# Kernel optimization log

Measured on AMD Instinct MI355X. Metric: run time of the kernel, lower is better.

Reference implementation:

```python
import jax, jax.numpy as jnp
import numpy as np

B, T, C = 2, 2048, 2048
H = 16
D = C // H  # head_size = 128
ROPE_BASE = 10000.0


def _rope_cos_sin(seq_len, dim, dtype=jnp.float32):
    # torchtune RotaryPositionalEmbeddings: interleaved pair rotation
    inv_freq = 1.0 / (ROPE_BASE ** (jnp.arange(0, dim, 2, dtype=jnp.float32) / dim))  # [D/2]
    ang = jnp.arange(seq_len, dtype=jnp.float32)[:, None] * inv_freq[None, :]  # [T, D/2]
    return jnp.cos(ang).astype(dtype), jnp.sin(ang).astype(dtype)


def _apply_rope(x, cos, sin):
    # x: [B, T, H, D]; rotate interleaved pairs (even, odd)
    x1 = x[..., 0::2]
    x2 = x[..., 1::2]
    c = cos[None, :, None, :]
    s = sin[None, :, None, :]
    out = jnp.stack([x1 * c - x2 * s, x1 * s + x2 * c], axis=-1)  # [B,T,H,D/2,2]
    return out.reshape(x.shape)


def setup_inputs() -> dict:
    key = jax.random.key(0)
    ks = jax.random.split(key, 5)
    scale = 1.0 / np.sqrt(C)
    return {
        "x": jax.random.normal(ks[0], (B, T, C), jnp.float32),
        "W_attn": jax.random.normal(ks[1], (C, 3 * C), jnp.float32) * scale,
        "b_attn": jax.random.normal(ks[2], (3 * C,), jnp.float32) * 0.01,
        "W_proj": jax.random.normal(ks[3], (C, C), jnp.float32) * scale,
        "b_proj": jax.random.normal(ks[4], (C,), jnp.float32) * 0.01,
    }


def reference(x, W_attn, b_attn, W_proj, b_proj):
    b, t, c = x.shape
    qkv = x @ W_attn + b_attn                      # [B,T,3C]
    q, k, v = jnp.split(qkv, 3, axis=-1)
    q = q.reshape(b, t, H, D)
    k = k.reshape(b, t, H, D)
    v = v.reshape(b, t, H, D)
    cos, sin = _rope_cos_sin(t, D, x.dtype)
    q = _apply_rope(q, cos, sin)
    k = _apply_rope(k, cos, sin)
    # [B,H,T,D]
    q = q.transpose(0, 2, 1, 3)
    k = k.transpose(0, 2, 1, 3)
    v = v.transpose(0, 2, 1, 3)
    scores = jnp.einsum("bhqd,bhkd->bhqk", q, k) / jnp.sqrt(jnp.asarray(D, x.dtype))
    causal = jnp.tril(jnp.ones((t, t), dtype=bool))  # [T,T]
    scores = jnp.where(causal[None, None], scores, jnp.asarray(-jnp.inf, scores.dtype))
    probs = jax.nn.softmax(scores, axis=-1)
    out = jnp.einsum("bhqk,bhkd->bhqd", probs, v)  # [B,H,T,D]
    out = out.transpose(0, 2, 1, 3).reshape(b, t, c)
    return out @ W_proj + b_proj
```

## Files before the change

kernel.cpp:

```cpp
#include <hip/hip_runtime.h>
#include <hip/hip_bf16.h>
#include <math.h>

#define B_ 2
#define T_ 2048
#define C_ 2048
#define H_ 16
#define D_ 128
#define M_ (B_ * T_)
#define N3C (3 * C_)

typedef __attribute__((ext_vector_type(8))) short v8s;
typedef __attribute__((ext_vector_type(4))) float v4f;

typedef const __attribute__((address_space(1))) void* gas_t;
typedef __attribute__((address_space(3))) void* las_t;

__device__ __forceinline__ void gl16(const void* g, void* l) {
  __builtin_amdgcn_global_load_lds((gas_t)g, (las_t)l, 16, 0, 0);
}
__device__ __forceinline__ v8s ldv(const unsigned short* p) { return *(const v8s*)p; }

__device__ inline unsigned short f2bf(float f) {
  unsigned u = __builtin_bit_cast(unsigned, f);
  u += 0x7FFFu + ((u >> 16) & 1u);
  return (unsigned short)(u >> 16);
}
__device__ inline float bf2f(unsigned short h) {
  unsigned u = (unsigned)h << 16;
  return __builtin_bit_cast(float, u);
}

__global__ __launch_bounds__(256) void split_rows(
    const float* __restrict__ X, unsigned short* __restrict__ XH,
    unsigned short* __restrict__ XL) {
  const long i4 = ((long)blockIdx.x * 256 + threadIdx.x) * 4;
  float4 v = *(const float4*)(X + i4);
  ushort4 hh, ll;
  hh.x = f2bf(v.x); ll.x = f2bf(v.x - bf2f(hh.x));
  hh.y = f2bf(v.y); ll.y = f2bf(v.y - bf2f(hh.y));
  hh.z = f2bf(v.z); ll.z = f2bf(v.z - bf2f(hh.z));
  hh.w = f2bf(v.w); ll.w = f2bf(v.w - bf2f(hh.w));
  *(ushort4*)&XH[i4] = hh;
  *(ushort4*)&XL[i4] = ll;
}

__global__ __launch_bounds__(256) void convert_wT(
    const float* __restrict__ W, unsigned short* __restrict__ WH,
    unsigned short* __restrict__ WL, int K, int N) {
  __shared__ float Ts[64][68];
  const int tid = threadIdx.x;
  const int n0 = blockIdx.x * 64;
  const int k0 = blockIdx.y * 64;
#pragma unroll
  for (int it = 0; it < 4; ++it) {
    int f = it * 256 + tid;
    int r = f >> 4;
    int c4 = (f & 15) * 4;
    float4 v = *(const float4*)(W + (long)(k0 + r) * N + n0 + c4);
    *(float4*)&Ts[r][c4] = v;
  }
  __syncthreads();
#pragma unroll
  for (int it = 0; it < 4; ++it) {
    int f = it * 256 + tid;
    int rn = f >> 4;
    int c4 = (f & 15) * 4;
    float x0 = Ts[c4 + 0][rn];
    float x1 = Ts[c4 + 1][rn];
    float x2 = Ts[c4 + 2][rn];
    float x3 = Ts[c4 + 3][rn];
    ushort4 hh, ll;
    hh.x = f2bf(x0); ll.x = f2bf(x0 - bf2f(hh.x));
    hh.y = f2bf(x1); ll.y = f2bf(x1 - bf2f(hh.y));
    hh.z = f2bf(x2); ll.z = f2bf(x2 - bf2f(hh.z));
    hh.w = f2bf(x3); ll.w = f2bf(x3 - bf2f(hh.w));
    long o = (long)(n0 + rn) * K + k0 + c4;
    *(ushort4*)&WH[o] = hh;
    *(ushort4*)&WL[o] = ll;
  }
}

__global__ __launch_bounds__(256) void gemm_pre_mfma(
    const unsigned short* __restrict__ AH, const unsigned short* __restrict__ AL,
    const unsigned short* __restrict__ BH, const unsigned short* __restrict__ BL,
    const float* __restrict__ bias, float* __restrict__ C, int K, int N) {
  __shared__ unsigned short smem[2 * 4 * 4096];

  const int tid = threadIdx.x;
  const int lane = tid & 63;
  const int w = tid >> 6;
  const int lm = lane & 15;
  const int quad = lane >> 4;

  const int gx = gridDim.x;
  const int lin = blockIdx.y * gx + blockIdx.x;
  const int pid_m = (lin & 7) + ((lin >> 3) / gx) * 8;
  const int pid_n = (lin >> 3) % gx;
  const int bm = pid_m * 128;
  const int bn = pid_n * 128;

  const int wm = (w & 1) * 64;
  const int wn = (w >> 1) * 64;

  const int srow = 32 * w + (lane >> 2);
  const int scol = ((lane & 3) ^ ((lane >> 3) & 3)) * 8;
  const unsigned short* pAH0 = AH + (size_t)(bm + srow) * K + scol;
  const unsigned short* pAH1 = pAH0 + (size_t)16 * K;
  const unsigned short* pAL0 = AL + (size_t)(bm + srow) * K + scol;
  const unsigned short* pAL1 = pAL0 + (size_t)16 * K;
  const unsigned short* pBH0 = BH + (size_t)(bn + srow) * K + scol;
  const unsigned short* pBH1 = pBH0 + (size_t)16 * K;
  const unsigned short* pBL0 = BL + (size_t)(bn + srow) * K + scol;
  const unsigned short* pBL1 = pBL0 + (size_t)16 * K;

#define STAGE(base, kk) do {                                      \
    unsigned short* d_ = (base) + 1024 * w;                       \
    const int ko_ = (kk) * 32;                                    \
    gl16(pAH0 + ko_, d_);                                         \
    gl16(pAH1 + ko_, d_ + 512);                                   \
    gl16(pAL0 + ko_, d_ + 4096);                                  \
    gl16(pAL1 + ko_, d_ + 4096 + 512);                            \
    gl16(pBH0 + ko_, d_ + 8192);                                  \
    gl16(pBH1 + ko_, d_ + 8192 + 512);                            \
    gl16(pBL0 + ko_, d_ + 12288);                                 \
    gl16(pBL1 + ko_, d_ + 12288 + 512);                           \
  } while (0)

  v4f acc[4][4];
#pragma unroll
  for (int i = 0; i < 4; ++i)
#pragma unroll
    for (int j = 0; j < 4; ++j) {
      v4f z = {0.f, 0.f, 0.f, 0.f};
      acc[i][j] = z;
    }

  const int kswz = (quad ^ ((lm >> 1) & 3)) * 8;

  const int nk = K >> 5;
  unsigned short* sb = smem;
  unsigned short* nb = smem + 16384;

  STAGE(sb, 0);

  for (int t = 0; t < nk; ++t) {
    __syncthreads();

    if (t + 1 < nk) STAGE(nb, t + 1);

    const unsigned short* sAH = sb;
    const unsigned short* sAL = sb + 4096;
    const unsigned short* sBH = sb + 8192;
    const unsigned short* sBL = sb + 12288;

    v8s aH[4], aL[4], bHf[4], bLf[4];
#pragma unroll
    for (int mt = 0; mt < 4; ++mt) {
      const int r = wm + mt * 16 + lm;
      aH[mt] = *(const v8s*)&sAH[r * 32 + kswz];
      aL[mt] = *(const v8s*)&sAL[r * 32 + kswz];
    }
#pragma unroll
    for (int nt = 0; nt < 4; ++nt) {
      const int r = wn + nt * 16 + lm;
      bHf[nt] = *(const v8s*)&sBH[r * 32 + kswz];
      bLf[nt] = *(const v8s*)&sBL[r * 32 + kswz];
    }

    __builtin_amdgcn_s_setprio(1);
#pragma unroll
    for (int mt = 0; mt < 4; ++mt)
#pragma unroll
      for (int nt = 0; nt < 4; ++nt) {
        acc[mt][nt] = __builtin_amdgcn_mfma_f32_16x16x32_bf16(aH[mt], bHf[nt], acc[mt][nt], 0, 0, 0);
        acc[mt][nt] = __builtin_amdgcn_mfma_f32_16x16x32_bf16(aH[mt], bLf[nt], acc[mt][nt], 0, 0, 0);
        acc[mt][nt] = __builtin_amdgcn_mfma_f32_16x16x32_bf16(aL[mt], bHf[nt], acc[mt][nt], 0, 0, 0);
      }
    __builtin_amdgcn_s_setprio(0);

    unsigned short* tmp = sb; sb = nb; nb = tmp;
  }
#undef STAGE

  __syncthreads();
  float* eps = (float*)smem;
  float* myeps = eps + w * 1088;

  float bv[4];
#pragma unroll
  for (int nt = 0; nt < 4; ++nt) bv[nt] = bias[bn + wn + nt * 16 + lm];

  const int r2 = lane >> 2;
  const int c4 = (lane & 3) * 4;
#pragma unroll
  for (int mt = 0; mt < 4; ++mt) {
#pragma unroll
    for (int nt = 0; nt < 4; ++nt)
#pragma unroll
      for (int r = 0; r < 4; ++r)
        myeps[(quad * 4 + r) * 68 + nt * 16 + lm] = acc[mt][nt][r] + bv[nt];
    float* dst = C + (size_t)(bm + wm + mt * 16 + r2) * N + bn + wn + c4;
#pragma unroll
    for (int i = 0; i < 4; ++i) {
      float4 v = *(float4*)&myeps[r2 * 68 + c4 + i * 16];
      *(float4*)&dst[i * 16] = v;
    }
  }
}

#define BAR() do { asm volatile("" ::: "memory"); __builtin_amdgcn_s_barrier(); asm volatile("" ::: "memory"); } while (0)

__global__ __launch_bounds__(512, 2) void gemm_qkv_8ph(
    const unsigned short* __restrict__ AH, const unsigned short* __restrict__ AL,
    const unsigned short* __restrict__ BH, const unsigned short* __restrict__ BL,
    const float* __restrict__ bias, float* __restrict__ C, int K, int N) {
  __shared__ unsigned short smem[2 * 28672];

  const int tid = threadIdx.x;
  const int lane = tid & 63;
  const int w = tid >> 6;
  const int lm = lane & 15;
  const int quad = lane >> 4;

  const int gx = gridDim.x;
  const int lin = blockIdx.y * gx + blockIdx.x;
  const int pid_m = (lin & 7) + ((lin >> 3) / gx) * 8;
  const int pid_n = (lin >> 3) % gx;
  const int bm = pid_m * 256;
  const int bn = pid_n * 192;

  const int wm = (w & 1) * 128;
  const int wn = (w >> 1) * 48;

  const unsigned short* aS[4]; int aD[4];
  {
    const int seg = tid >> 8;
    const int rr = (tid & 255) >> 2;
    const int cc = tid & 3;
#pragma unroll
    for (int j = 0; j < 4; ++j) {
      int row = (j >> 1) * 64 + seg * 128 + rr;
      int pl = j & 1;
      int c = cc ^ ((row >> 1) & 3);
      aS[j] = (pl ? AL : AH) + (size_t)(bm + row) * K + c * 8;
      aD[j] = pl * 8192 + row * 32 + cc * 8;
    }
  }
  const unsigned short* bS[3]; int bD[3];
#pragma unroll
  for (int j = 0; j < 3; ++j) {
    int g = tid + 512 * j;
    int pl = (g >= 768) ? 1 : 0;
    int p = g - pl * 768;
    int row = p >> 2;
    int c = (p & 3) ^ ((row >> 1) & 3);
    bS[j] = (pl ? BL : BH) + (size_t)(bn + row) * K + c * 8;
    bD[j] = 16384 + pl * 6144 + p * 8;
  }

  v4f acc[8][3];
#pragma unroll
  for (int i = 0; i < 8; ++i)
#pragma unroll
    for (int j = 0; j < 3; ++j) {
      v4f z = {0.f, 0.f, 0.f, 0.f};
      acc[i][j] = z;
    }

  const int kswz = (quad ^ ((lm >> 1) & 3)) * 8;
  const int nk = K >> 5;

  gl16(bS[0], smem + bD[0]);
  gl16(bS[1], smem + bD[1]);
  gl16(bS[2], smem + bD[2]);
  gl16(aS[0], smem + aD[0]);
  gl16(aS[1], smem + aD[1]);
  gl16(aS[2], smem + aD[2]);
  gl16(aS[3], smem + aD[3]);

#define MM3(MT, NT, AH_, AL_)                                                           \
  acc[MT][NT] = __builtin_amdgcn_mfma_f32_16x16x32_bf16(AH_, bh##NT, acc[MT][NT], 0, 0, 0); \
  acc[MT][NT] = __builtin_amdgcn_mfma_f32_16x16x32_bf16(AH_, bl##NT, acc[MT][NT], 0, 0, 0); \
  acc[MT][NT] = __builtin_amdgcn_mfma_f32_16x16x32_bf16(AL_, bh##NT, acc[MT][NT], 0, 0, 0);
#define MROW(MT, XH_, XL_) MM3(MT, 0, XH_, XL_) MM3(MT, 1, XH_, XL_) MM3(MT, 2, XH_, XL_)
#define AFRAG(MT) ldv(sbuf + (wm + (MT) * 16 + lm) * 32 + kswz)
#define AFRAGL(MT) ldv(sbuf + 8192 + (wm + (MT) * 16 + lm) * 32 + kswz)

  for (int t = 0; t < nk; ++t) {
    const unsigned short* sbuf = smem + (t & 1) * 28672;
    unsigned short* nbuf = (unsigned short*)smem + ((t + 1) & 1) * 28672;
    const int kn = (t + 1) * 32;
    const bool pf = (t + 1 < nk);

    if (pf) {
      gl16(bS[0] + kn, nbuf + bD[0]);
      gl16(bS[1] + kn, nbuf + bD[1]);
      gl16(bS[2] + kn, nbuf + bD[2]);
      asm volatile("s_waitcnt vmcnt(5)" ::: "memory");
    } else {
      asm volatile("s_waitcnt vmcnt(2)" ::: "memory");
    }
    BAR();

    v8s bh0 = ldv(sbuf + 16384 + (wn + lm) * 32 + kswz);
    v8s bl0 = ldv(sbuf + 22528 + (wn + lm) * 32 + kswz);
    v8s bh1 = ldv(sbuf + 16384 + (wn + 16 + lm) * 32 + kswz);
    v8s bl1 = ldv(sbuf + 22528 + (wn + 16 + lm) * 32 + kswz);
    v8s bh2 = ldv(sbuf + 16384 + (wn + 32 + lm) * 32 + kswz);
    v8s bl2 = ldv(sbuf + 22528 + (wn + 32 + lm) * 32 + kswz);
    {
      v8s x0h = AFRAG(0), x0l = AFRAGL(0);
      v8s x1h = AFRAG(1), x1l = AFRAGL(1);
      v8s x2h = AFRAG(2), x2l = AFRAGL(2);
      v8s x3h = AFRAG(3), x3l = AFRAGL(3);
      __builtin_amdgcn_s_setprio(1);
      MROW(0, x0h, x0l)
      MROW(1, x1h, x1l)
      __builtin_amdgcn_s_setprio(0);
      if (pf) {
        gl16(aS[0] + kn, nbuf + aD[0]);
        gl16(aS[1] + kn, nbuf + aD[1]);
      }
      __builtin_amdgcn_s_setprio(1);
      MROW(2, x2h, x2l)
      MROW(3, x3h, x3l)
      __builtin_amdgcn_s_setprio(0);
    }

    if (pf) {
      gl16(aS[2] + kn, nbuf + aD[2]);
      gl16(aS[3] + kn, nbuf + aD[3]);
      asm volatile("s_waitcnt vmcnt(7)" ::: "memory");
    } else {
      asm volatile("s_waitcnt vmcnt(0)" ::: "memory");
    }
    BAR();

    {
      v8s x4h = AFRAG(4), x4l = AFRAGL(4);
      v8s x5h = AFRAG(5), x5l = AFRAGL(5);
      v8s x6h = AFRAG(6), x6l = AFRAGL(6);
      v8s x7h = AFRAG(7), x7l = AFRAGL(7);
      __builtin_amdgcn_s_setprio(1);
      MROW(4, x4h, x4l)
      MROW(5, x5h, x5l)
      MROW(6, x6h, x6l)
      MROW(7, x7h, x7l)
      __builtin_amdgcn_s_setprio(0);
    }
    BAR();
  }
#undef AFRAGL
#undef AFRAG
#undef MROW
#undef MM3

  __syncthreads();
  float* eps = (float*)smem;
  float* myeps = eps + w * 1088;

  float bv[3];
#pragma unroll
  for (int nt = 0; nt < 3; ++nt) bv[nt] = bias[bn + wn + nt * 16 + lm];

  const int r2 = lane >> 2;
  const int c4 = (lane & 3) * 4;
#pragma unroll
  for (int mt = 0; mt < 8; ++mt) {
#pragma unroll
    for (int nt = 0; nt < 3; ++nt)
#pragma unroll
      for (int r = 0; r < 4; ++r)
        myeps[(quad * 4 + r) * 68 + nt * 16 + lm] = acc[mt][nt][r] + bv[nt];
    float* dst = C + (size_t)(bm + wm + mt * 16 + r2) * N + bn + wn + c4;
#pragma unroll
    for (int i = 0; i < 3; ++i) {
      float4 v = *(float4*)&myeps[r2 * 68 + c4 + i * 16];
      *(float4*)&dst[i * 16] = v;
    }
  }
}

__global__ __launch_bounds__(256) void rope_split(
    const float* __restrict__ qkv,
    unsigned short* __restrict__ QH, unsigned short* __restrict__ QL,
    unsigned short* __restrict__ KH, unsigned short* __restrict__ KL,
    unsigned short* __restrict__ VTH, unsigned short* __restrict__ VTL) {
  const int tb = blockIdx.x;
  const int h = blockIdx.y;
  const int b = blockIdx.z;
  const int tid = threadIdx.x;

  __shared__ unsigned short VH_s[128][66];
  __shared__ unsigned short VL_s[128][66];

  for (int part = 0; part < 2; ++part) {
    unsigned short* OH = part ? KH : QH;
    unsigned short* OL = part ? KL : QL;
    const float sc = part ? 1.0f : 0.12751879523595298f;
    const size_t colbase = (size_t)part * C_ + (size_t)h * D_;
#pragma unroll 2
    for (int it = 0; it < 16; ++it) {
      int f = it * 256 + tid;
      int r = f >> 6;
      int i = f & 63;
      int t = tb * 64 + r;
      float inv = exp2f(-(float)i * (13.28771237954945f / 64.0f));
      float ang = (float)t * inv;
      float s, c;
      sincosf(ang, &s, &c);
      const float* src = qkv + (size_t)(b * T_ + t) * N3C + colbase + 2 * i;
      float2 x = *(const float2*)src;
      float ox = (x.x * c - x.y * s) * sc;
      float oy = (x.x * s + x.y * c) * sc;
      size_t dst = ((size_t)(b * H_ + h) * T_ + t) * D_ + 2 * i;
      unsigned short hx = f2bf(ox), hy = f2bf(oy);
      ushort2 hh; hh.x = hx; hh.y = hy;
      *(ushort2*)&OH[dst] = hh;
      ushort2 ll; ll.x = f2bf(ox - bf2f(hx)); ll.y = f2bf(oy - bf2f(hy));
      *(ushort2*)&OL[dst] = ll;
    }
  }

#pragma unroll
  for (int it = 0; it < 8; ++it) {
    int f = it * 256 + tid;
    int r = f >> 5;
    int d4 = (f & 31) * 4;
    float4 v = *(const float4*)(qkv + (size_t)(b * T_ + tb * 64 + r) * N3C + 2 * C_ + h * D_ + d4);
    float vv[4] = {v.x, v.y, v.z, v.w};
#pragma unroll
    for (int j = 0; j < 4; ++j) {
      unsigned short hi = f2bf(vv[j]);
      VH_s[d4 + j][r] = hi;
      VL_s[d4 + j][r] = f2bf(vv[j] - bf2f(hi));
    }
  }
  __syncthreads();
#pragma unroll
  for (int it = 0; it < 4; ++it) {
    int f = it * 256 + tid;
    int d = f >> 3;
    int c8 = (f & 7) * 8;
    size_t dst = ((size_t)(b * H_ + h) * D_ + d) * T_ + tb * 64 + c8;
    unsigned short th[8], tl[8];
#pragma unroll
    for (int j = 0; j < 8; ++j) { th[j] = VH_s[d][c8 + j]; tl[j] = VL_s[d][c8 + j]; }
    *(uint4*)&VTH[dst] = *(uint4*)th;
    *(uint4*)&VTL[dst] = *(uint4*)tl;
  }
}

__global__ __launch_bounds__(512, 4) void attn_mfma(
    const unsigned short* __restrict__ QH, const unsigned short* __restrict__ QL,
    const unsigned short* __restrict__ KH, const unsigned short* __restrict__ KL,
    const unsigned short* __restrict__ VTH, const unsigned short* __restrict__ VTL,
    unsigned short* __restrict__ OHp, unsigned short* __restrict__ OLp) {
  const int qb = (int)gridDim.x - 1 - (int)blockIdx.x;
  const int h = blockIdx.y;
  const int b = blockIdx.z;
  const int tid = threadIdx.x;
  const int lane = tid & 63;
  const int w = tid >> 6;
  const int lm = lane & 15;
  const int quad = lane >> 4;

  __shared__ unsigned short KS_H[32][136], KS_L[32][136];
  __shared__ unsigned short VS_H[128][40], VS_L[128][40];
  __shared__ unsigned short PS_H[128][40], PS_L[128][40];

  const size_t qbase = ((size_t)(b * H_ + h) * T_ + qb * 128 + w * 16 + lm) * D_;
  v8s qh[4], ql[4];
#pragma unroll
  for (int ks = 0; ks < 4; ++ks) {
    qh[ks] = *(const v8s*)&QH[qbase + ks * 32 + quad * 8];
    ql[ks] = *(const v8s*)&QL[qbase + ks * 32 + quad * 8];
  }

  v8s ones;
#pragma unroll
  for (int j = 0; j < 8; ++j) ones[j] = (short)0x3F80;

  const int kr = tid >> 4;
  const int kc = (tid & 15) * 8;
  const int vd = tid >> 2;
  const int vc = (tid & 3) * 8;

  const size_t kbase0 = (size_t)(b * H_ + h) * T_ * D_;
  const size_t vbase0 = (size_t)(b * H_ + h) * D_ * T_;
  const int nkb = 4 * qb + 4;

  uint4 khp = *(const uint4*)&KH[kbase0 + (size_t)kr * D_ + kc];
  uint4 klp = *(const uint4*)&KL[kbase0 + (size_t)kr * D_ + kc];
  uint4 vhp = *(const uint4*)&VTH[vbase0 + (size_t)vd * T_ + vc];
  uint4 vlp = *(const uint4*)&VTL[vbase0 + (size_t)vd * T_ + vc];

  v4f acc_o[8], acc_l;
#pragma unroll
  for (int nt = 0; nt < 8; ++nt) {
    v4f z = {0.f, 0.f, 0.f, 0.f};
    acc_o[nt] = z;
  }
  {
    v4f z = {0.f, 0.f, 0.f, 0.f};
    acc_l = z;
  }

  const float M2 = 32.0f;

  for (int kb = 0; kb < nkb; ++kb) {
    __syncthreads();
    *(uint4*)&KS_H[kr][kc] = khp;
    *(uint4*)&KS_L[kr][kc] = klp;
    *(uint4*)&VS_H[vd][vc] = vhp;
    *(uint4*)&VS_L[vd][vc] = vlp;
    __syncthreads();

    if (kb + 1 < nkb) {
      size_t kg = kbase0 + (size_t)((kb + 1) * 32 + kr) * D_ + kc;
      khp = *(const uint4*)&KH[kg];
      klp = *(const uint4*)&KL[kg];
      size_t vg = vbase0 + (size_t)vd * T_ + (kb + 1) * 32 + vc;
      vhp = *(const uint4*)&VTH[vg];
      vlp = *(const uint4*)&VTL[vg];
    }

    v4f s0, s1;
    {
      v4f z = {0.f, 0.f, 0.f, 0.f};
      s0 = z; s1 = z;
    }
#pragma unroll
    for (int ks = 0; ks < 4; ++ks) {
      int k8 = ks * 32 + quad * 8;
      v8s bh0 = *(const v8s*)&KS_H[lm][k8];
      v8s bl0 = *(const v8s*)&KS_L[lm][k8];
      v8s bh1 = *(const v8s*)&KS_H[16 + lm][k8];
      v8s bl1 = *(const v8s*)&KS_L[16 + lm][k8];
      s0 = __builtin_amdgcn_mfma_f32_16x16x32_bf16(qh[ks], bh0, s0, 0, 0, 0);
      s1 = __builtin_amdgcn_mfma_f32_16x16x32_bf16(qh[ks], bh1, s1, 0, 0, 0);
      s0 = __builtin_amdgcn_mfma_f32_16x16x32_bf16(qh[ks], bl0, s0, 0, 0, 0);
      s1 = __builtin_amdgcn_mfma_f32_16x16x32_bf16(qh[ks], bl1, s1, 0, 0, 0);
      s0 = __builtin_amdgcn_mfma_f32_16x16x32_bf16(ql[ks], bh0, s0, 0, 0, 0);
      s1 = __builtin_amdgcn_mfma_f32_16x16x32_bf16(ql[ks], bh1, s1, 0, 0, 0);
    }

#pragma unroll
    for (int r = 0; r < 4; ++r) {
      int rowg = qb * 128 + w * 16 + quad * 4 + r;
      float v0 = (kb * 32 + lm > rowg) ? -INFINITY : s0[r];
      float v1 = (kb * 32 + 16 + lm > rowg) ? -INFINITY : s1[r];
      float p0 = __builtin_amdgcn_exp2f(v0 - M2);
      float p1 = __builtin_amdgcn_exp2f(v1 - M2);

      int prow = w * 16 + quad * 4 + r;
      unsigned short p0h = f2bf(p0);
      PS_H[prow][lm] = p0h;
      PS_L[prow][lm] = f2bf(p0 - bf2f(p0h));
      unsigned short p1h = f2bf(p1);
      PS_H[prow][16 + lm] = p1h;
      PS_L[prow][16 + lm] = f2bf(p1 - bf2f(p1h));
    }

    v8s ph = *(const v8s*)&PS_H[w * 16 + lm][quad * 8];
    v8s pl = *(const v8s*)&PS_L[w * 16 + lm][quad * 8];
    acc_l = __builtin_amdgcn_mfma_f32_16x16x32_bf16(ph, ones, acc_l, 0, 0, 0);
    acc_l = __builtin_amdgcn_mfma_f32_16x16x32_bf16(pl, ones, acc_l, 0, 0, 0);
#pragma unroll
    for (int nt = 0; nt < 8; ++nt) {
      v8s vh = *(const v8s*)&VS_H[nt * 16 + lm][quad * 8];
      v8s vl = *(const v8s*)&VS_L[nt * 16 + lm][quad * 8];
      acc_o[nt] = __builtin_amdgcn_mfma_f32_16x16x32_bf16(ph, vh, acc_o[nt], 0, 0, 0);
      acc_o[nt] = __builtin_amdgcn_mfma_f32_16x16x32_bf16(ph, vl, acc_o[nt], 0, 0, 0);
      acc_o[nt] = __builtin_amdgcn_mfma_f32_16x16x32_bf16(pl, vh, acc_o[nt], 0, 0, 0);
    }
  }

#pragma unroll
  for (int r = 0; r < 4; ++r) {
    float invl = 1.0f / acc_l[r];
    size_t row = (size_t)(b * T_ + qb * 128 + w * 16 + quad * 4 + r);
#pragma unroll
    for (int nt = 0; nt < 8; ++nt) {
      float o = acc_o[nt][r] * invl;
      unsigned short oh = f2bf(o);
      size_t idx = row * C_ + h * D_ + nt * 16 + lm;
      OHp[idx] = oh;
      OLp[idx] = f2bf(o - bf2f(oh));
    }
  }
}

extern "C" void kernel_launch(void* const* d_in, const int* in_sizes, int n_in,
                              void* d_out, int out_size, void* d_ws, size_t ws_size,
                              hipStream_t stream) {
  const float* x      = (const float*)d_in[0];
  const float* W_attn = (const float*)d_in[1];
  const float* b_attn = (const float*)d_in[2];
  const float* W_proj = (const float*)d_in[3];
  const float* b_proj = (const float*)d_in[4];
  float* out = (float*)d_out;

  char* wsb = (char*)d_ws;
  const size_t MiB = 1048576;
  float* qkv = (float*)wsb;
  unsigned short* WtaH = (unsigned short*)(wsb + 96 * MiB);
  unsigned short* WtaL = (unsigned short*)(wsb + 120 * MiB);
  unsigned short* XH   = (unsigned short*)(wsb + 144 * MiB);
  unsigned short* XL   = (unsigned short*)(wsb + 160 * MiB);
  unsigned short* QH   = (unsigned short*)(wsb + 96 * MiB);
  unsigned short* QL   = (unsigned short*)(wsb + 112 * MiB);
  unsigned short* KH   = (unsigned short*)(wsb + 128 * MiB);
  unsigned short* KL   = (unsigned short*)(wsb + 144 * MiB);
  unsigned short* VTH  = (unsigned short*)(wsb + 160 * MiB);
  unsigned short* VTL  = (unsigned short*)(wsb + 176 * MiB);
  unsigned short* WtpH = (unsigned short*)(wsb + 32 * MiB);
  unsigned short* WtpL = (unsigned short*)(wsb + 40 * MiB);
  unsigned short* AOH  = (unsigned short*)(wsb + 48 * MiB);
  unsigned short* AOL  = (unsigned short*)(wsb + 64 * MiB);

  convert_wT<<<dim3(N3C / 64, C_ / 64), 256, 0, stream>>>(W_attn, WtaH, WtaL, C_, N3C);
  split_rows<<<dim3((M_ * C_) / 1024), 256, 0, stream>>>(x, XH, XL);
  gemm_qkv_8ph<<<dim3(N3C / 192, M_ / 256), 512, 0, stream>>>(
      XH, XL, WtaH, WtaL, b_attn, qkv, C_, N3C);
  rope_split<<<dim3(T_ / 64, H_, B_), 256, 0, stream>>>(qkv, QH, QL, KH, KL, VTH, VTL);
  convert_wT<<<dim3(C_ / 64, C_ / 64), 256, 0, stream>>>(W_proj, WtpH, WtpL, C_, C_);
  attn_mfma<<<dim3(T_ / 128, H_, B_), 512, 0, stream>>>(
      QH, QL, KH, KL, VTH, VTL, AOH, AOL);
  gemm_pre_mfma<<<dim3(C_ / 128, M_ / 128), 256, 0, stream>>>(
      AOH, AOL, WtpH, WtpL, b_proj, out, C_, C_);
}
```

Before: 711.8 us.

## Fuse RoPE and hi/lo bf16 split into QKV GEMM epilogue

The separate rope_split kernel is removed. The QKV GEMM epilogue now applies rotary embedding and scaling to Q/K and writes split bf16 hi/lo outputs directly, transposing V with scattered 2-byte stores. This avoids writing and re-reading the 96 MiB fp32 qkv intermediate and one kernel launch. The cost is extra transcendental work in the GEMM epilogue and uncoalesced strided stores for the V transpose. The workspace layout is also reshuffled.

```diff
diff --git a/kernel.cpp b/kernel.cpp
--- a/kernel.cpp
+++ b/kernel.cpp
@@ -214,7 +214,11 @@
 __global__ __launch_bounds__(512, 2) void gemm_qkv_8ph(
     const unsigned short* __restrict__ AH, const unsigned short* __restrict__ AL,
     const unsigned short* __restrict__ BH, const unsigned short* __restrict__ BL,
-    const float* __restrict__ bias, float* __restrict__ C, int K, int N) {
+    const float* __restrict__ bias,
+    unsigned short* __restrict__ QH, unsigned short* __restrict__ QL,
+    unsigned short* __restrict__ KH, unsigned short* __restrict__ KL,
+    unsigned short* __restrict__ VTH, unsigned short* __restrict__ VTL,
+    int K, int N) {
   __shared__ unsigned short smem[2 * 28672];
 
   const int tid = threadIdx.x;
@@ -366,6 +370,8 @@
 
   const int r2 = lane >> 2;
   const int c4 = (lane & 3) * 4;
+  const float RC = 13.28771237954945f / 64.0f;
+
 #pragma unroll
   for (int mt = 0; mt < 8; ++mt) {
 #pragma unroll
@@ -373,82 +379,53 @@
 #pragma unroll
       for (int r = 0; r < 4; ++r)
         myeps[(quad * 4 + r) * 68 + nt * 16 + lm] = acc[mt][nt][r] + bv[nt];
-    float* dst = C + (size_t)(bm + wm + mt * 16 + r2) * N + bn + wn + c4;
+
+    const int row = bm + wm + mt * 16 + r2;
+    const int bb = row >> 11;
+    const int tt = row & 2047;
 #pragma unroll
     for (int i = 0; i < 3; ++i) {
       float4 v = *(float4*)&myeps[r2 * 68 + c4 + i * 16];
-      *(float4*)&dst[i * 16] = v;
-    }
-  }
-}
-
-__global__ __launch_bounds__(256) void rope_split(
-    const float* __restrict__ qkv,
-    unsigned short* __restrict__ QH, unsigned short* __restrict__ QL,
-    unsigned short* __restrict__ KH, unsigned short* __restrict__ KL,
-    unsigned short* __restrict__ VTH, unsigned short* __restrict__ VTL) {
-  const int tb = blockIdx.x;
-  const int h = blockIdx.y;
-  const int b = blockIdx.z;
-  const int tid = threadIdx.x;
-
-  __shared__ unsigned short VH_s[128][66];
-  __shared__ unsigned short VL_s[128][66];
-
-  for (int part = 0; part < 2; ++part) {
-    unsigned short* OH = part ? KH : QH;
-    unsigned short* OL = part ? KL : QL;
-    const float sc = part ? 1.0f : 0.12751879523595298f;
-    const size_t colbase = (size_t)part * C_ + (size_t)h * D_;
-#pragma unroll 2
-    for (int it = 0; it < 16; ++it) {
-      int f = it * 256 + tid;
-      int r = f >> 6;
-      int i = f & 63;
-      int t = tb * 64 + r;
-      float inv = exp2f(-(float)i * (13.28771237954945f / 64.0f));
-      float ang = (float)t * inv;
-      float s, c;
-      sincosf(ang, &s, &c);
-      const float* src = qkv + (size_t)(b * T_ + t) * N3C + colbase + 2 * i;
-      float2 x = *(const float2*)src;
-      float ox = (x.x * c - x.y * s) * sc;
-      float oy = (x.x * s + x.y * c) * sc;
-      size_t dst = ((size_t)(b * H_ + h) * T_ + t) * D_ + 2 * i;
-      unsigned short hx = f2bf(ox), hy = f2bf(oy);
-      ushort2 hh; hh.x = hx; hh.y = hy;
-      *(ushort2*)&OH[dst] = hh;
-      ushort2 ll; ll.x = f2bf(ox - bf2f(hx)); ll.y = f2bf(oy - bf2f(hy));
-      *(ushort2*)&OL[dst] = ll;
-    }
-  }
-
-#pragma unroll
-  for (int it = 0; it < 8; ++it) {
-    int f = it * 256 + tid;
-    int r = f >> 5;
-    int d4 = (f & 31) * 4;
-    float4 v = *(const float4*)(qkv + (size_t)(b * T_ + tb * 64 + r) * N3C + 2 * C_ + h * D_ + d4);
-    float vv[4] = {v.x, v.y, v.z, v.w};
-#pragma unroll
-    for (int j = 0; j < 4; ++j) {
-      unsigned short hi = f2bf(vv[j]);
-      VH_s[d4 + j][r] = hi;
-      VL_s[d4 + j][r] = f2bf(vv[j] - bf2f(hi));
-    }
-  }
-  __syncthreads();
-#pragma unroll
-  for (int it = 0; it < 4; ++it) {
-    int f = it * 256 + tid;
-    int d = f >> 3;
-    int c8 = (f & 7) * 8;
-    size_t dst = ((size_t)(b * H_ + h) * D_ + d) * T_ + tb * 64 + c8;
-    unsigned short th[8], tl[8];
-#pragma unroll
-    for (int j = 0; j < 8; ++j) { th[j] = VH_s[d][c8 + j]; tl[j] = VL_s[d][c8 + j]; }
-    *(uint4*)&VTH[dst] = *(uint4*)th;
-    *(uint4*)&VTL[dst] = *(uint4*)tl;
+      const int col = bn + wn + c4 + i * 16;
+      const int part = col >> 11;
+      const int cc = col & 2047;
+      const int hh = cc >> 7;
+      const int d0 = cc & 127;
+      if (part < 2) {
+        const float sc = part ? 1.0f : 0.12751879523595298f;
+        const int ip = d0 >> 1;
+        float inv0 = exp2f(-(float)ip * RC);
+        float inv1 = exp2f(-(float)(ip + 1) * RC);
+        float s0, c0, s1, c1;
+        sincosf((float)tt * inv0, &s0, &c0);
+        sincosf((float)tt * inv1, &s1, &c1);
+        float ox0 = (v.x * c0 - v.y * s0) * sc;
+        float oy0 = (v.x * s0 + v.y * c0) * sc;
+        float ox1 = (v.z * c1 - v.w * s1) * sc;
+        float oy1 = (v.z * s1 + v.w * c1) * sc;
+        unsigned short h0 = f2bf(ox0), h1 = f2bf(oy0);
+        unsigned short h2 = f2bf(ox1), h3 = f2bf(oy1);
+        ushort4 hv; hv.x = h0; hv.y = h1; hv.z = h2; hv.w = h3;
+        ushort4 lv;
+        lv.x = f2bf(ox0 - bf2f(h0)); lv.y = f2bf(oy0 - bf2f(h1));
+        lv.z = f2bf(ox1 - bf2f(h2)); lv.w = f2bf(oy1 - bf2f(h3));
+        unsigned short* OH = part ? KH : QH;
+        unsigned short* OL = part ? KL : QL;
+        size_t dst = ((size_t)(bb * H_ + hh) * T_ + tt) * D_ + d0;
+        *(ushort4*)&OH[dst] = hv;
+        *(ushort4*)&OL[dst] = lv;
+      } else {
+        size_t vb = (size_t)(bb * H_ + hh) * D_;
+        float vv[4] = {v.x, v.y, v.z, v.w};
+#pragma unroll
+        for (int j = 0; j < 4; ++j) {
+          unsigned short hv = f2bf(vv[j]);
+          size_t dst = (vb + d0 + j) * T_ + tt;
+          VTH[dst] = hv;
+          VTL[dst] = f2bf(vv[j] - bf2f(hv));
+        }
+      }
+    }
   }
 }
 
@@ -604,27 +581,25 @@
 
   char* wsb = (char*)d_ws;
   const size_t MiB = 1048576;
-  float* qkv = (float*)wsb;
-  unsigned short* WtaH = (unsigned short*)(wsb + 96 * MiB);
-  unsigned short* WtaL = (unsigned short*)(wsb + 120 * MiB);
-  unsigned short* XH   = (unsigned short*)(wsb + 144 * MiB);
-  unsigned short* XL   = (unsigned short*)(wsb + 160 * MiB);
-  unsigned short* QH   = (unsigned short*)(wsb + 96 * MiB);
-  unsigned short* QL   = (unsigned short*)(wsb + 112 * MiB);
-  unsigned short* KH   = (unsigned short*)(wsb + 128 * MiB);
-  unsigned short* KL   = (unsigned short*)(wsb + 144 * MiB);
-  unsigned short* VTH  = (unsigned short*)(wsb + 160 * MiB);
-  unsigned short* VTL  = (unsigned short*)(wsb + 176 * MiB);
-  unsigned short* WtpH = (unsigned short*)(wsb + 32 * MiB);
-  unsigned short* WtpL = (unsigned short*)(wsb + 40 * MiB);
-  unsigned short* AOH  = (unsigned short*)(wsb + 48 * MiB);
-  unsigned short* AOL  = (unsigned short*)(wsb + 64 * MiB);
+  unsigned short* XH   = (unsigned short*)(wsb + 0 * MiB);
+  unsigned short* XL   = (unsigned short*)(wsb + 16 * MiB);
+  unsigned short* WtaH = (unsigned short*)(wsb + 32 * MiB);
+  unsigned short* WtaL = (unsigned short*)(wsb + 56 * MiB);
+  unsigned short* QH   = (unsigned short*)(wsb + 80 * MiB);
+  unsigned short* QL   = (unsigned short*)(wsb + 96 * MiB);
+  unsigned short* KH   = (unsigned short*)(wsb + 112 * MiB);
+  unsigned short* KL   = (unsigned short*)(wsb + 128 * MiB);
+  unsigned short* VTH  = (unsigned short*)(wsb + 144 * MiB);
+  unsigned short* VTL  = (unsigned short*)(wsb + 160 * MiB);
+  unsigned short* WtpH = (unsigned short*)(wsb + 0 * MiB);
+  unsigned short* WtpL = (unsigned short*)(wsb + 8 * MiB);
+  unsigned short* AOH  = (unsigned short*)(wsb + 32 * MiB);
+  unsigned short* AOL  = (unsigned short*)(wsb + 48 * MiB);
 
   convert_wT<<<dim3(N3C / 64, C_ / 64), 256, 0, stream>>>(W_attn, WtaH, WtaL, C_, N3C);
   split_rows<<<dim3((M_ * C_) / 1024), 256, 0, stream>>>(x, XH, XL);
   gemm_qkv_8ph<<<dim3(N3C / 192, M_ / 256), 512, 0, stream>>>(
-      XH, XL, WtaH, WtaL, b_attn, qkv, C_, N3C);
-  rope_split<<<dim3(T_ / 64, H_, B_), 256, 0, stream>>>(qkv, QH, QL, KH, KL, VTH, VTL);
+      XH, XL, WtaH, WtaL, b_attn, QH, QL, KH, KL, VTH, VTL, C_, N3C);
   convert_wT<<<dim3(C_ / 64, C_ / 64), 256, 0, stream>>>(W_proj, WtpH, WtpL, C_, C_);
   attn_mfma<<<dim3(T_ / 128, H_, B_), 512, 0, stream>>>(
       QH, QL, KH, KL, VTH, VTL, AOH, AOL);
```

Measured after the change: 737.1 us. 3.6% more time.
